# Optimization experiments

Measured on AMD Instinct MI355X. Metric: run time of the kernel, lower is better.

## Reference

```python
import jax, jax.numpy as jnp
import numpy as np

B, H_IMG, W_IMG, C_IMG, NP = 8, 384, 384, 3, 6
DELTA = 10
TOL = 1e-3
LAM = 0.05          # lambda_ (Charbonnier scale)
MAX_ITER = 12
RIDGE = 1e-6


def _cubic(s):
    # Keys bicubic convolution kernel, a = -0.5
    a = -0.5
    s = jnp.abs(s)
    s2 = s * s
    s3 = s2 * s
    w1 = (a + 2.0) * s3 - (a + 3.0) * s2 + 1.0
    w2 = a * s3 - 5.0 * a * s2 + 8.0 * a * s - 4.0 * a
    return jnp.where(s <= 1.0, w1, jnp.where(s < 2.0, w2, 0.0))


def _bicubic(I, xg, yg):
    # I: [b,H,W,C]; xg,yg: [b,H,W] sample coordinates
    Bn, Hh, Ww, C = I.shape
    x0 = jnp.floor(xg)
    y0 = jnp.floor(yg)
    tx = xg - x0
    ty = yg - y0
    xi = x0.astype(jnp.int32)
    yi = y0.astype(jnp.int32)
    bidx = jnp.arange(Bn)[:, None, None]
    out = jnp.zeros(I.shape, I.dtype)
    for j in range(4):           # fixed 4x4 tap stencil
        wy = _cubic(ty - (j - 1))
        yy = jnp.clip(yi + (j - 1), 0, Hh - 1)
        for k in range(4):
            wx = _cubic(tx - (k - 1))
            xx = jnp.clip(xi + (k - 1), 0, Ww - 1)
            out = out + (wy * wx)[..., None] * I[bidx, yy, xx, :]
    return out


def _params2matrix(p):
    # AFFINITY: x' = x + p0 + p2*x + p3*y ; y' = y + p1 + p4*x + p5*y
    zero = jnp.zeros_like(p[:, 0])
    one = jnp.ones_like(p[:, 0])
    r0 = jnp.stack([1.0 + p[:, 2], p[:, 3], p[:, 0]], -1)
    r1 = jnp.stack([p[:, 4], 1.0 + p[:, 5], p[:, 1]], -1)
    r2 = jnp.stack([zero, zero, one], -1)
    return jnp.stack([r0, r1, r2], 1)


def _matrix2params(M):
    M = M / M[:, 2:3, 2:3]
    return jnp.stack([M[:, 0, 2], M[:, 1, 2], M[:, 0, 0] - 1.0,
                      M[:, 0, 1], M[:, 1, 0], M[:, 1, 1] - 1.0], -1)


def _gradients(I):
    # central differences, zero-padded at the borders (as in compute_gradients)
    Ix = jnp.pad((I[:, :, 2:, :] - I[:, :, :-2, :]) * 0.5,
                 ((0, 0), (0, 0), (1, 1), (0, 0)))
    Iy = jnp.pad((I[:, 2:, :, :] - I[:, :-2, :, :]) * 0.5,
                 ((0, 0), (1, 1), (0, 0), (0, 0)))
    return Ix, Iy


def setup_inputs() -> dict:
    key = jax.random.key(0)
    k1, k2 = jax.random.split(key)
    I1 = jax.random.uniform(k1, (B, H_IMG, W_IMG, C_IMG), jnp.float32)
    I2 = jax.random.uniform(k2, (B, H_IMG, W_IMG, C_IMG), jnp.float32)
    p = jnp.zeros((B, NP), jnp.float32)
    return {"I1": I1, "I2": I2, "p": p}


def _forward(I1, I2, p):
    Bn, Hh, Ww, C = I1.shape
    x = jnp.arange(Ww, dtype=jnp.float32)
    y = jnp.arange(Hh, dtype=jnp.float32)
    X, Y = jnp.meshgrid(x, y)
    ones = jnp.ones_like(X)
    zeros = jnp.zeros_like(X)
    # AFFINITY Jacobian, split into Jx / Jy halves: [H,W,6]
    Jx = jnp.stack([ones, zeros, X, Y, zeros, zeros], -1)
    Jy = jnp.stack([zeros, ones, zeros, zeros, X, Y], -1)
    Ix, Iy = _gradients(I1)
    # steepest-descent images: [b,H,W,C,6]
    DIJ = Ix[..., None] * Jx[None, :, :, None, :] + Iy[..., None] * Jy[None, :, :, None, :]
    rows_ok = (jnp.arange(Hh) >= DELTA) & (jnp.arange(Hh) < Hh - DELTA)
    cols_ok = (jnp.arange(Ww) >= DELTA) & (jnp.arange(Ww) < Ww - DELTA)
    valid1 = (rows_ok[:, None] & cols_ok[None, :])[None, :, :, None]  # [1,H,W,1]
    coords = jnp.stack([X, Y, ones], 0)  # [3,H,W]
    eye = jnp.eye(NP, dtype=jnp.float32)

    def warp(pcur):
        M = _params2matrix(pcur)
        g = jnp.einsum('bij,jhw->bihw', M, coords)
        xg, yg = g[:, 0], g[:, 1]
        Iw = _bicubic(I2, xg, yg)
        gx = jnp.round(xg).astype(jnp.int32)
        gy = jnp.round(yg).astype(jnp.int32)
        wmask = ((gx >= DELTA) & (gx <= Ww - DELTA) &
                 (gy >= DELTA) & (gy <= Hh - DELTA))[..., None]
        return Iw, wmask

    def step(carry, _):
        pcur, done = carry
        Iw, wmask = carry_warp = warp(pcur)
        m = wmask & valid1
        DI = jnp.where(m, Iw - I1, 0.0)
        # Charbonnier influence weight psi(e) = 1/sqrt(1 + (e/lam)^2)
        w = jnp.where(m, jax.lax.rsqrt(1.0 + (DI / LAM) ** 2), 0.0)
        bvec = jnp.einsum('bhwcm,bhwc->bm', DIJ, w * DI)
        Hm = jnp.einsum('bhwcm,bhwcn->bmn', DIJ * w[..., None], DIJ)
        dp = jnp.linalg.solve(Hm + RIDGE * eye, bvec[..., None])[..., 0]
        # inverse-compositional update: W(p) <- W(p) o W(dp)^-1
        Mn = _params2matrix(pcur) @ jnp.linalg.inv(_params2matrix(dp))
        p_new = _matrix2params(Mn)
        conv = jnp.linalg.norm(dp, axis=-1) < TOL
        p_out = jnp.where(done[:, None], pcur, p_new)
        return (p_out, done | conv), None

    (pf, _), _ = jax.lax.scan(step, (p, jnp.zeros((Bn,), bool)), None, length=MAX_ITER)
    Iw, wmask = warp(pf)
    m = wmask & valid1
    DI = jnp.where(m, Iw - I1, 0.0)
    rho = 2.0 * LAM * LAM * (jnp.sqrt(1.0 + (DI / LAM) ** 2) - 1.0)
    mb = jnp.broadcast_to(m, DI.shape)
    cnt = jnp.sum(mb.astype(jnp.float32), axis=(1, 2, 3))
    err = jnp.sum(jnp.where(mb, rho, 0.0), axis=(1, 2, 3)) / jnp.maximum(cnt, 1.0)
    return pf, err, DI, Iw


def reference(I1, I2, p):
    return _forward(I1, I2, p)
```

## Files before the change

### kernel.cpp

```cpp
#include <hip/hip_runtime.h>
#include <math.h>

#define BB 8
#define HH 384
#define WW 384
#define NPAR 6
#define DEL 10
#define MAXIT 12
#define NACC 24
#define HWPIX (HH*WW)
#define NRT4 91
#define PITCH2 195
#define NR2 8
#define WS2C 194
#define WIN 182
#define PITCHF 141
#define WSF 140
#define KB_ 8
#define SPS 32

typedef float vf4 __attribute__((ext_vector_type(4)));
typedef vf4 uvf4 __attribute__((aligned(4)));
typedef float f2v __attribute__((ext_vector_type(2), aligned(4)));
typedef float lf4 __attribute__((ext_vector_type(4)));

__device__ __forceinline__ vf4 ldv4(const float* p) { return *(const uvf4*)p; }

__device__ __forceinline__ lf4 ldpx3(const float* __restrict__ Ib, int pixoff) {
    const int fo = pixoff * 3;
    if (fo + 4 <= HWPIX * 3) {
        vf4 v = ldv4(Ib + fo);
        return (lf4){v.x, v.y, v.z, 0.f};
    }
    vf4 v = ldv4(Ib + fo - 1);
    return (lf4){v.y, v.z, v.w, 0.f};
}

__device__ __forceinline__ float cubicw(float s) {
    s = fabsf(s);
    float s2 = s * s, s3 = s2 * s;
    float w1 = 1.5f * s3 - 2.5f * s2 + 1.0f;
    float w2 = -0.5f * s3 + 2.5f * s2 - 4.0f * s + 2.0f;
    return (s <= 1.0f) ? w1 : ((s < 2.0f) ? w2 : 0.0f);
}

__device__ __forceinline__ void bicubic3_fast(const float* __restrict__ Ib, double xg, double yg, float Iw[3]) {
    double fx = floor(xg), fy = floor(yg);
    float tx = (float)(xg - fx), ty = (float)(yg - fy);
    int xi = (int)fx, yi = (int)fy;
    float wx[4], wyv[4];
#pragma unroll
    for (int k = 0; k < 4; k++) { wx[k] = cubicw(tx - (float)(k - 1)); wyv[k] = cubicw(ty - (float)(k - 1)); }
    Iw[0] = 0.f; Iw[1] = 0.f; Iw[2] = 0.f;
    const float* base = Ib + (yi - 1) * (WW * 3) + (xi - 1) * 3;
#pragma unroll
    for (int j = 0; j < 4; j++) {
        const float* r = base + j * (WW * 3);
        vf4 v0 = ldv4(r), v1 = ldv4(r + 4), v2 = ldv4(r + 8);
        float r0 = fmaf(wx[0], v0.x, 0.f); r0 = fmaf(wx[1], v0.w, r0); r0 = fmaf(wx[2], v1.z, r0); r0 = fmaf(wx[3], v2.y, r0);
        float r1 = fmaf(wx[0], v0.y, 0.f); r1 = fmaf(wx[1], v1.x, r1); r1 = fmaf(wx[2], v1.w, r1); r1 = fmaf(wx[3], v2.z, r1);
        float r2 = fmaf(wx[0], v0.z, 0.f); r2 = fmaf(wx[1], v1.y, r2); r2 = fmaf(wx[2], v2.x, r2); r2 = fmaf(wx[3], v2.w, r2);
        Iw[0] = fmaf(wyv[j], r0, Iw[0]);
        Iw[1] = fmaf(wyv[j], r1, Iw[1]);
        Iw[2] = fmaf(wyv[j], r2, Iw[2]);
    }
}

__device__ __forceinline__ void bicubic3_gen(const float* __restrict__ Ib, double xg, double yg, float Iw[3]) {
    double fx = floor(xg), fy = floor(yg);
    int xi = (int)fx, yi = (int)fy;
    float tx = (float)(xg - fx), ty = (float)(yg - fy);
    float wx[4], wyv[4];
    int xx[4], yy[4];
#pragma unroll
    for (int k = 0; k < 4; k++) {
        wx[k] = cubicw(tx - (float)(k - 1)); wyv[k] = cubicw(ty - (float)(k - 1));
        xx[k] = min(max(xi + k - 1, 0), WW - 1);
        yy[k] = min(max(yi + k - 1, 0), HH - 1);
    }
    Iw[0] = 0.f; Iw[1] = 0.f; Iw[2] = 0.f;
#pragma unroll
    for (int j = 0; j < 4; j++) {
        const float* row = Ib + yy[j] * (WW * 3);
        float r0 = 0.f, r1 = 0.f, r2 = 0.f;
#pragma unroll
        for (int k = 0; k < 4; k++) {
            const float* q = row + xx[k] * 3;
            r0 = fmaf(wx[k], q[0], r0); r1 = fmaf(wx[k], q[1], r1); r2 = fmaf(wx[k], q[2], r2);
        }
        Iw[0] = fmaf(wyv[j], r0, Iw[0]);
        Iw[1] = fmaf(wyv[j], r1, Iw[1]);
        Iw[2] = fmaf(wyv[j], r2, Iw[2]);
    }
}

template<int P>
__device__ __forceinline__ void bicubic3_lds(const lf4* __restrict__ T, int ssx, int ssy,
                                             float tx, float ty, float Iw[3]) {
    float wx[4], wyv[4];
#pragma unroll
    for (int k = 0; k < 4; k++) { wx[k] = cubicw(tx - (float)(k - 1)); wyv[k] = cubicw(ty - (float)(k - 1)); }
    Iw[0] = 0.f; Iw[1] = 0.f; Iw[2] = 0.f;
    const lf4* bp = T + (ssy - 1) * P + (ssx - 1);
#pragma unroll
    for (int j = 0; j < 4; j++) {
        lf4 t0 = bp[j * P + 0], t1 = bp[j * P + 1], t2 = bp[j * P + 2], t3 = bp[j * P + 3];
        float r0 = fmaf(wx[0], t0.x, 0.f); r0 = fmaf(wx[1], t1.x, r0); r0 = fmaf(wx[2], t2.x, r0); r0 = fmaf(wx[3], t3.x, r0);
        float r1 = fmaf(wx[0], t0.y, 0.f); r1 = fmaf(wx[1], t1.y, r1); r1 = fmaf(wx[2], t2.y, r1); r1 = fmaf(wx[3], t3.y, r1);
        float r2 = fmaf(wx[0], t0.z, 0.f); r2 = fmaf(wx[1], t1.z, r2); r2 = fmaf(wx[2], t2.z, r2); r2 = fmaf(wx[3], t3.z, r2);
        Iw[0] = fmaf(wyv[j], r0, Iw[0]);
        Iw[1] = fmaf(wyv[j], r1, Iw[1]);
        Iw[2] = fmaf(wyv[j], r2, Iw[2]);
    }
}

__device__ __forceinline__
void solve6_fast(const double* __restrict__ Sb, const double* __restrict__ pc,
                 double pn[6], int* convp) {
    const double b0 = Sb[0], b1 = Sb[3], b2 = Sb[1], b3 = Sb[2], b4 = Sb[4], b5 = Sb[5];
    const double h00 = Sb[6]  + 1e-6, h01 = Sb[12], h02 = Sb[7],  h03 = Sb[8],  h04 = Sb[13], h05 = Sb[14];
    const double h11 = Sb[18] + 1e-6, h12 = Sb[13], h13 = Sb[14], h14 = Sb[19], h15 = Sb[20];
    const double h22 = Sb[9]  + 1e-6, h23 = Sb[10], h24 = Sb[15], h25 = Sb[16];
    const double h33 = Sb[11] + 1e-6, h34 = Sb[16], h35 = Sb[17];
    const double h44 = Sb[21] + 1e-6, h45 = Sb[22];
    const double h55 = Sb[23] + 1e-6;

    const double l00 = sqrt(h00);
    const double i0 = 1.0 / l00;
    const double l10 = h01 * i0, l20 = h02 * i0, l30 = h03 * i0, l40 = h04 * i0, l50 = h05 * i0;
    const double l11 = sqrt(h11 - l10 * l10);
    const double i1 = 1.0 / l11;
    const double l21 = (h12 - l20 * l10) * i1;
    const double l31 = (h13 - l30 * l10) * i1;
    const double l41 = (h14 - l40 * l10) * i1;
    const double l51 = (h15 - l50 * l10) * i1;
    const double l22 = sqrt(h22 - l20 * l20 - l21 * l21);
    const double i2 = 1.0 / l22;
    const double l32 = (h23 - l30 * l20 - l31 * l21) * i2;
    const double l42 = (h24 - l40 * l20 - l41 * l21) * i2;
    const double l52 = (h25 - l50 * l20 - l51 * l21) * i2;
    const double l33 = sqrt(h33 - l30 * l30 - l31 * l31 - l32 * l32);
    const double i3 = 1.0 / l33;
    const double l43 = (h34 - l40 * l30 - l41 * l31 - l42 * l32) * i3;
    const double l53 = (h35 - l50 * l30 - l51 * l31 - l52 * l32) * i3;
    const double l44 = sqrt(h44 - l40 * l40 - l41 * l41 - l42 * l42 - l43 * l43);
    const double i4 = 1.0 / l44;
    const double l54 = (h45 - l50 * l40 - l51 * l41 - l52 * l42 - l53 * l43) * i4;
    const double l55 = sqrt(h55 - l50 * l50 - l51 * l51 - l52 * l52 - l53 * l53 - l54 * l54);
    const double i5 = 1.0 / l55;

    const double y0 = b0 * i0;
    const double y1 = (b1 - l10 * y0) * i1;
    const double y2 = (b2 - l20 * y0 - l21 * y1) * i2;
    const double y3 = (b3 - l30 * y0 - l31 * y1 - l32 * y2) * i3;
    const double y4 = (b4 - l40 * y0 - l41 * y1 - l42 * y2 - l43 * y3) * i4;
    const double y5 = (b5 - l50 * y0 - l51 * y1 - l52 * y2 - l53 * y3 - l54 * y4) * i5;

    const double d5 = y5 * i5;
    const double d4 = (y4 - l54 * d5) * i4;
    const double d3 = (y3 - l43 * d4 - l53 * d5) * i3;
    const double d2 = (y2 - l32 * d3 - l42 * d4 - l52 * d5) * i2;
    const double d1 = (y1 - l21 * d2 - l31 * d3 - l41 * d4 - l51 * d5) * i1;
    const double d0 = (y0 - l10 * d1 - l20 * d2 - l30 * d3 - l40 * d4 - l50 * d5) * i0;

    const double nrm = sqrt(d0*d0 + d1*d1 + d2*d2 + d3*d3 + d4*d4 + d5*d5);
    *convp = (nrm < 1e-3) ? 1 : 0;

    const double m00 = 1.0 + pc[2], m01 = pc[3], m02 = pc[0];
    const double m10 = pc[4], m11 = 1.0 + pc[5], m12 = pc[1];
    const double q00 = 1.0 + d2, q01 = d3, q02 = d0;
    const double q10 = d4, q11 = 1.0 + d5, q12 = d1;
    const double det = q00 * q11 - q01 * q10;
    const double j00 = q11 / det, j01 = -q01 / det;
    const double j10 = -q10 / det, j11 = q00 / det;
    const double jt0 = -(j00 * q02 + j01 * q12);
    const double jt1 = -(j10 * q02 + j11 * q12);
    const double n00 = m00 * j00 + m01 * j10;
    const double n01 = m00 * j01 + m01 * j11;
    const double n02 = m00 * jt0 + m01 * jt1 + m02;
    const double n10 = m10 * j00 + m11 * j10;
    const double n11 = m10 * j01 + m11 * j11;
    const double n12 = m10 * jt0 + m11 * jt1 + m12;
    pn[0] = n02;
    pn[1] = n12;
    pn[2] = n00 - 1.0;
    pn[3] = n01;
    pn[4] = n10;
    pn[5] = n11 - 1.0;
}

extern "C" __global__ __launch_bounds__(256)
void k_init(const float* __restrict__ p0, double* __restrict__ p_store,
            int* __restrict__ done0, double* __restrict__ S_part_all,
            double* __restrict__ Sf_part) {
    const int idx = blockIdx.x * 256 + threadIdx.x;
    const int n = MAXIT * KB_ * BB * SPS;
    for (int i = idx; i < n; i += gridDim.x * 256) S_part_all[i] = 0.0;
    if (blockIdx.x == 0) {
        const int tid = threadIdx.x;
        if (tid < KB_ * BB * 4) Sf_part[tid] = 0.0;
        if (tid < BB * NPAR) p_store[tid] = (double)p0[tid];
        if (tid < BB) done0[tid] = 0;
    }
}

extern "C" __global__ __launch_bounds__(256)
void k_iter(const float* __restrict__ I1, const float* __restrict__ I2,
            const double* __restrict__ p_in, const int* __restrict__ done_in,
            const double* __restrict__ S_in, double* __restrict__ S_out,
            double* __restrict__ p_out_g, int* __restrict__ done_out_g,
            int first) {
    __shared__ lf4 SMEM[NR2 * PITCH2];
    __shared__ double Ssum[NACC];
    __shared__ double pbc[NPAR];
    __shared__ int dbc;
    const int tid = threadIdx.x;
    const int b = blockIdx.y;

    if (!first) {
        if (tid < NACC) {
            double a0 = 0.0, a1 = 0.0;
#pragma unroll
            for (int k = 0; k < KB_; k += 2) {
                a0 += S_in[((size_t)(k * BB + b)) * SPS + tid];
                a1 += S_in[((size_t)((k + 1) * BB + b)) * SPS + tid];
            }
            Ssum[tid] = a0 + a1;
        }
        __syncthreads();
    }
    if (tid == 0) {
        if (first) {
#pragma unroll
            for (int i = 0; i < NPAR; i++) pbc[i] = p_in[b * NPAR + i];
            dbc = done_in[b];
        } else {
            if (done_in[b]) {
#pragma unroll
                for (int i = 0; i < NPAR; i++) pbc[i] = p_in[b * NPAR + i];
                dbc = 1;
            } else {
                double pn[6]; int conv;
                solve6_fast(Ssum, p_in + b * NPAR, pn, &conv);
#pragma unroll
                for (int i = 0; i < NPAR; i++) pbc[i] = pn[i];
                dbc = conv;
            }
            if (blockIdx.x == 0) {
#pragma unroll
                for (int i = 0; i < NPAR; i++) p_out_g[b * NPAR + i] = pbc[i];
                done_out_g[b] = dbc;
            }
        }
    }
    __syncthreads();
    if (dbc) return;

    const int tix = blockIdx.x;
    const int rt = tix >> 1, win = tix & 1;
    const int y0 = 10 + rt * 4;
    const int x0 = 10 + win * WIN;
    const int sx0 = x0 - 6;

    const double M00 = 1.0 + pbc[2], M01 = pbc[3], M02 = pbc[0];
    const double M10 = pbc[4], M11 = 1.0 + pbc[5], M12 = pbc[1];
    const float* I1b = I1 + (size_t)b * HWPIX * 3;
    const float* I2b = I2 + (size_t)b * HWPIX * 3;

    const double ygc = M10 * (double)(x0 + 91) + M11 * ((double)y0 + 1.5) + M12;
    const int r0 = (int)fmin(fmax(floor(ygc) - 3.0, -100000.0), 100000.0);

    for (int i = tid; i < NR2 * WS2C; i += 256) {
        const int r = i / WS2C, c = i - r * WS2C;
        const int gr = min(max(r0 + r, 0), HH - 1);
        const int gc = min(sx0 + c, WW - 1);
        SMEM[r * PITCH2 + c] = ldpx3(I2b, gr * WW + gc);
    }
    __syncthreads();

    const int wid = tid >> 6, lane = tid & 63;
    const int y = y0 + wid;
    const double Y = (double)y;
    const double Bx = M01 * Y + M02;
    const double By = M11 * Y + M12;

    double s[13];
#pragma unroll
    for (int i = 0; i < 13; i++) s[i] = 0.0;

#pragma unroll
    for (int step = 0; step < 3; step++) {
        const int col = lane + 64 * step;
        const int x = x0 + col;
        const double X = (double)x;
        const double xg = fma(M00, X, Bx);
        const double yg = fma(M10, X, By);
        const double gx = rint(xg), gy = rint(yg);
        const bool ok = (col < WIN) &&
                        (gx >= (double)DEL && gx <= (double)(WW - DEL) &&
                         gy >= (double)DEL && gy <= (double)(HH - DEL));
        const double fx = floor(xg), fy = floor(yg);
        const int xi = (int)fx, yi = (int)fy;
        const float tx = (float)(xg - fx), ty = (float)(yg - fy);
        const int sxi = xi - sx0, syi = yi - r0;
        const bool inwin = ok && (sxi >= 1) && (sxi <= WS2C - 3) && (syi >= 1) && (syi <= NR2 - 3);

        float Iw[3];
        if (ok && !inwin) {
            bicubic3_fast(I2b, xg, yg, Iw);
        } else {
            const int ssx = inwin ? sxi : 8;
            const int ssy = inwin ? syi : 2;
            bicubic3_lds<PITCH2>(SMEM, ssx, ssy, tx, ty, Iw);
        }

        const int xc = min(x, WW - DEL - 1);
        const int pixL = y * WW + xc;
        const float* c = I1b + pixL * 3;
        vf4 u0 = ldv4(c - 3);
        vf4 u1 = ldv4(c + 1);
        float cr2 = c[5];
        vf4 uu = ldv4(c - WW * 3);
        vf4 ud = ldv4(c + WW * 3);

        const float cl[3] = {u0.x, u0.y, u0.z};
        const float cv[3] = {u0.w, u1.x, u1.y};
        const float cr[3] = {u1.z, u1.w, cr2};
        const float cu[3] = {uu.x, uu.y, uu.z};
        const float cd[3] = {ud.x, ud.y, ud.z};

        const float msk = ok ? 1.0f : 0.0f;
        float Af = 0.f, Bf = 0.f, Cf = 0.f, T0f = 0.f, T1f = 0.f;
#pragma unroll
        for (int ch = 0; ch < 3; ch++) {
            const float Ix = (cr[ch] - cl[ch]) * 0.5f;
            const float Iy = (cd[ch] - cu[ch]) * 0.5f;
            const float d = Iw[ch] - cv[ch];
            const float u = d * 20.0f;
            const float w = msk / sqrtf(fmaf(u, u, 1.0f));
            const float wd = w * d;
            T0f = fmaf(Ix, wd, T0f);
            T1f = fmaf(Iy, wd, T1f);
            const float wIx = w * Ix;
            Af = fmaf(wIx, Ix, Af);
            Bf = fmaf(wIx, Iy, Bf);
            Cf = fmaf(w * Iy, Iy, Cf);
        }
        const double T0 = (double)T0f, T1 = (double)T1f;
        const double A = (double)Af, Bd = (double)Bf, Cd = (double)Cf;
        const double XX = X * X;
        s[0] += T0;  s[1] = fma(T0, X, s[1]);
        s[2] += T1;  s[3] = fma(T1, X, s[3]);
        s[4] += A;   s[5] = fma(A, X, s[5]);   s[6] = fma(A, XX, s[6]);
        s[7] += Bd;  s[8] = fma(Bd, X, s[8]);  s[9] = fma(Bd, XX, s[9]);
        s[10] += Cd; s[11] = fma(Cd, X, s[11]); s[12] = fma(Cd, XX, s[12]);
    }

#pragma unroll
    for (int i = 0; i < 13; i++) s[i] += __shfl_down(s[i], 32, 64);

    __syncthreads();
    double* scr = (double*)SMEM;
    if (lane < 32) {
        double* o = scr + ((size_t)(wid * 32 + lane)) * 13;
#pragma unroll
        for (int i = 0; i < 13; i++) o[i] = s[i];
    }
    __syncthreads();

    if (tid < NACC) {
        const int comp[NACC] = {0,1,0, 2,3,2, 4,5,4, 6,5,4, 7,8,7, 9,8,7, 10,11,10, 12,11,10};
        const int ypw[NACC]  = {0,0,1, 0,0,1, 0,0,1, 0,1,2, 0,0,1, 0,1,2, 0,0,1,   0,1,2};
        const int cix = comp[tid], pw = ypw[tid];
        double acc = 0.0;
        for (int w = 0; w < 4; w++) {
            const double* basep = scr + ((size_t)(w * 32)) * 13 + cix;
            double part = 0.0;
            for (int l = 0; l < 32; l++) part += basep[(size_t)l * 13];
            const double Yw = (double)(y0 + w);
            const double f = (pw == 0) ? 1.0 : ((pw == 1) ? Yw : Yw * Yw);
            acc = fma(f, part, acc);
        }
        const int bkt = blockIdx.x & (KB_ - 1);
        unsafeAtomicAdd(&S_out[((size_t)(bkt * BB + b)) * SPS + tid], acc);
    }
}

extern "C" __global__ __launch_bounds__(256)
void k_final_map(const float* __restrict__ I1, const float* __restrict__ I2,
                 const double* __restrict__ p_in, const int* __restrict__ done_in,
                 const double* __restrict__ S_in, double* __restrict__ pf_g,
                 float* __restrict__ DI_out, float* __restrict__ Iw_out,
                 double* __restrict__ Sf_part) {
    __shared__ lf4 I2S[NR2 * PITCHF];
    __shared__ double wsum[4][2];
    __shared__ double Ssum[NACC];
    __shared__ double pbc[NPAR];
    const int tid = threadIdx.x;
    const int b = blockIdx.y;

    if (tid < NACC) {
        double a0 = 0.0, a1 = 0.0;
#pragma unroll
        for (int k = 0; k < KB_; k += 2) {
            a0 += S_in[((size_t)(k * BB + b)) * SPS + tid];
            a1 += S_in[((size_t)((k + 1) * BB + b)) * SPS + tid];
        }
        Ssum[tid] = a0 + a1;
    }
    __syncthreads();
    if (tid == 0) {
        if (done_in[b]) {
#pragma unroll
            for (int i = 0; i < NPAR; i++) pbc[i] = p_in[b * NPAR + i];
        } else {
            double pn[6]; int conv;
            solve6_fast(Ssum, p_in + b * NPAR, pn, &conv);
#pragma unroll
            for (int i = 0; i < NPAR; i++) pbc[i] = pn[i];
        }
        if (blockIdx.x == 0) {
#pragma unroll
            for (int i = 0; i < NPAR; i++) pf_g[b * NPAR + i] = pbc[i];
        }
    }
    __syncthreads();

    const int tix = blockIdx.x;
    const int rt = tix / 3, win = tix - rt * 3;
    const int y0 = rt * 4;
    const int x0 = win * 128;
    const int sx0 = x0 - 6;

    const double M00 = 1.0 + pbc[2], M01 = pbc[3], M02 = pbc[0];
    const double M10 = pbc[4], M11 = 1.0 + pbc[5], M12 = pbc[1];
    const float* I1b = I1 + (size_t)b * HWPIX * 3;
    const float* I2b = I2 + (size_t)b * HWPIX * 3;
    float* DIb = DI_out + (size_t)b * HWPIX * 3;
    float* Iwb = Iw_out + (size_t)b * HWPIX * 3;

    const double ygc = M10 * (double)(x0 + 64) + M11 * ((double)y0 + 1.5) + M12;
    const int r0 = (int)fmin(fmax(floor(ygc) - 3.0, -100000.0), 100000.0);

    for (int i = tid; i < NR2 * WSF; i += 256) {
        const int r = i / WSF, c = i - r * WSF;
        const int gr = min(max(r0 + r, 0), HH - 1);
        const int gc = min(max(sx0 + c, 0), WW - 1);
        I2S[r * PITCHF + c] = ldpx3(I2b, gr * WW + gc);
    }
    __syncthreads();

    const int row = tid >> 6, lane = tid & 63;
    const int y = y0 + row;
    const int x1 = x0 + 2 * lane;
    const int pix1 = y * WW + x1;

    float Iwp[2][3];
    bool mp[2];
    double rho_s = 0.0, cnt_s = 0.0;

    const float* cbase = I1b + (size_t)pix1 * 3;
    const vf4 Ac = ldv4(cbase);
    const vf4 A2c = ldv4(cbase + 2);

#pragma unroll
    for (int j = 0; j < 2; j++) {
        const int x = x1 + j;
        const double X = (double)x, Yd = (double)y;
        const double xg = fma(M00, X, fma(M01, Yd, M02));
        const double yg = fma(M10, X, fma(M11, Yd, M12));
        const double fx = floor(xg), fy = floor(yg);
        const int xi = (int)fx, yi = (int)fy;
        const float tx = (float)(xg - fx), ty = (float)(yg - fy);
        const int sxi = xi - sx0, syi = yi - r0;
        const bool inwin = (sxi >= 1) && (sxi <= WSF - 3) && (syi >= 1) && (syi <= NR2 - 3);

        if (inwin) bicubic3_lds<PITCHF>(I2S, sxi, syi, tx, ty, Iwp[j]);
        else       bicubic3_gen(I2b, xg, yg, Iwp[j]);

        const bool v1 = (x >= DEL) && (x < WW - DEL) && (y >= DEL) && (y < HH - DEL);
        const double gx = rint(xg), gy = rint(yg);
        const bool wm = (gx >= (double)DEL && gx <= (double)(WW - DEL) &&
                         gy >= (double)DEL && gy <= (double)(HH - DEL));
        mp[j] = v1 && wm;
    }

    {
        float* wp = Iwb + (size_t)pix1 * 3;
        *(uvf4*)wp = (vf4){Iwp[0][0], Iwp[0][1], Iwp[0][2], Iwp[1][0]};
        *(f2v*)(wp + 4) = (f2v){Iwp[1][1], Iwp[1][2]};
    }
    {
        const float cv1[3] = {Ac.x, Ac.y, Ac.z};
        const float cv2[3] = {Ac.w, A2c.z, A2c.w};
        float dv[6];
#pragma unroll
        for (int ch = 0; ch < 3; ch++) {
            const float d1 = mp[0] ? (Iwp[0][ch] - cv1[ch]) : 0.0f;
            const float d2 = mp[1] ? (Iwp[1][ch] - cv2[ch]) : 0.0f;
            dv[ch] = d1;
            dv[3 + ch] = d2;
            if (mp[0]) {
                const float u = d1 * 20.0f;
                rho_s += (double)(0.005f * (sqrtf(fmaf(u, u, 1.0f)) - 1.0f));
            }
            if (mp[1]) {
                const float u = d2 * 20.0f;
                rho_s += (double)(0.005f * (sqrtf(fmaf(u, u, 1.0f)) - 1.0f));
            }
        }
        if (mp[0]) cnt_s += 3.0;
        if (mp[1]) cnt_s += 3.0;
        float* dp_ = DIb + (size_t)pix1 * 3;
        *(uvf4*)dp_ = (vf4){dv[0], dv[1], dv[2], dv[3]};
        *(f2v*)(dp_ + 4) = (f2v){dv[4], dv[5]};
    }

#pragma unroll
    for (int off = 32; off >= 1; off >>= 1) {
        rho_s += __shfl_down(rho_s, off, 64);
        cnt_s += __shfl_down(cnt_s, off, 64);
    }
    if (lane == 0) { wsum[row][0] = rho_s; wsum[row][1] = cnt_s; }
    __syncthreads();
    if (tid < 2) {
        double sv = wsum[0][tid] + wsum[1][tid] + wsum[2][tid] + wsum[3][tid];
        const int bkt = blockIdx.x & (KB_ - 1);
        unsafeAtomicAdd(&Sf_part[((size_t)(bkt * BB + b)) * 4 + tid], sv);
    }
}

extern "C" __global__ void k_finish(const double* __restrict__ p_fin,
                                    const double* __restrict__ Sf_part,
                                    float* __restrict__ out) {
    const int tid = threadIdx.x;
    if (tid < BB * NPAR) out[tid] = (float)p_fin[tid];
    if (tid >= 48 && tid < 48 + BB) {
        const int b = tid - 48;
        double rs = 0.0, cs = 0.0;
#pragma unroll
        for (int k = 0; k < KB_; k++) {
            rs += Sf_part[((size_t)(k * BB + b)) * 4 + 0];
            cs += Sf_part[((size_t)(k * BB + b)) * 4 + 1];
        }
        out[48 + b] = (float)(rs / fmax(cs, 1.0));
    }
}

extern "C" void kernel_launch(void* const* d_in, const int* in_sizes, int n_in,
                              void* d_out, int out_size, void* d_ws, size_t ws_size,
                              hipStream_t stream) {
    const float* I1 = (const float*)d_in[0];
    const float* I2 = (const float*)d_in[1];
    const float* p0 = (const float*)d_in[2];
    float* out = (float*)d_out;

    double* p_store = (double*)d_ws;
    int* done_flags = (int*)((char*)d_ws + 4992);
    double* S_part_all = (double*)((char*)d_ws + 5408);
    double* Sf_part = (double*)((char*)d_ws + 202016);

    k_init<<<8, 256, 0, stream>>>(p0, p_store, done_flags, S_part_all, Sf_part);

    const size_t SIT = (size_t)KB_ * BB * SPS;
    dim3 gridI(NRT4 * 2, BB), blkI(256);
    for (int it = 0; it < MAXIT; it++) {
        const int first = (it == 0) ? 1 : 0;
        const double* p_in = p_store + (size_t)(first ? 0 : (it - 1)) * BB * NPAR;
        const int* d_in_f = done_flags + (first ? 0 : (it - 1)) * BB;
        const double* S_in = S_part_all + (size_t)(first ? 0 : (it - 1)) * SIT;
        k_iter<<<gridI, blkI, 0, stream>>>(I1, I2, p_in, d_in_f, S_in,
                                           S_part_all + (size_t)it * SIT,
                                           p_store + (size_t)it * BB * NPAR,
                                           done_flags + it * BB, first);
    }
    float* DI_out = out + 56;
    float* Iw_out = out + 56 + (size_t)BB * HWPIX * 3;
    dim3 gridF(96 * 3, BB), blkF(256);
    k_final_map<<<gridF, blkF, 0, stream>>>(I1, I2,
                                            p_store + (size_t)11 * BB * NPAR,
                                            done_flags + 11 * BB,
                                            S_part_all + (size_t)11 * SIT,
                                            p_store + (size_t)MAXIT * BB * NPAR,
                                            DI_out, Iw_out, Sf_part);
    k_finish<<<1, 64, 0, stream>>>(p_store + (size_t)MAXIT * BB * NPAR, Sf_part, out);
}
```

Before: 425.5 us.

## Retile iteration and final kernels to one pixel per thread, prefetch warp source early

```diff
diff --git a/kernel.cpp b/kernel.cpp
--- a/kernel.cpp
+++ b/kernel.cpp
@@ -10,10 +10,11 @@
 #define NACC 24
 #define HWPIX (HH*WW)
 #define NRT4 91
-#define PITCH2 195
 #define NR2 8
-#define WS2C 194
-#define WIN 182
+#define W_STG 76
+#define PITCH2 77
+#define NWIN 6
+#define NR2F 6
 #define PITCHF 141
 #define WSF 140
 #define KB_ 8
@@ -204,40 +205,64 @@
     }
 }
 
-extern "C" __global__ __launch_bounds__(256)
+extern "C" __global__ __launch_bounds__(256, 8)
 void k_iter(const float* __restrict__ I1, const float* __restrict__ I2,
             const double* __restrict__ p_in, const int* __restrict__ done_in,
             const double* __restrict__ S_in, double* __restrict__ S_out,
             double* __restrict__ p_out_g, int* __restrict__ done_out_g,
             int first) {
-    __shared__ lf4 SMEM[NR2 * PITCH2];
+    __shared__ __align__(16) double SMEMD[1664];
     __shared__ double Ssum[NACC];
     __shared__ double pbc[NPAR];
     __shared__ int dbc;
+    lf4* SMEM = (lf4*)SMEMD;
     const int tid = threadIdx.x;
     const int b = blockIdx.y;
-
-    if (!first) {
-        if (tid < NACC) {
-            double a0 = 0.0, a1 = 0.0;
-#pragma unroll
-            for (int k = 0; k < KB_; k += 2) {
-                a0 += S_in[((size_t)(k * BB + b)) * SPS + tid];
-                a1 += S_in[((size_t)((k + 1) * BB + b)) * SPS + tid];
-            }
-            Ssum[tid] = a0 + a1;
-        }
-        __syncthreads();
-    }
+    const int tix = blockIdx.x;
+    const int rt = tix / NWIN, win = tix - rt * NWIN;
+    const int y0 = 10 + rt * 4;
+    const int x0 = 10 + win * 64;
+    const int sx0 = x0 - 6;
+
+    double pp[NPAR];
+#pragma unroll
+    for (int i = 0; i < NPAR; i++) pp[i] = p_in[b * NPAR + i];
+    {
+        const double pM10 = pp[4], pM11 = 1.0 + pp[5], pM12 = pp[1];
+        const double ygc = pM10 * (double)(x0 + 32) + pM11 * ((double)y0 + 1.5) + pM12;
+        const int r0 = (int)fmin(fmax(floor(ygc) - 3.0, -100000.0), 100000.0);
+        const float* I2b = I2 + (size_t)b * HWPIX * 3;
+        for (int i = tid; i < NR2 * W_STG; i += 256) {
+            const int r = i / W_STG, c = i - r * W_STG;
+            const int gr = min(max(r0 + r, 0), HH - 1);
+            const int gc = min(sx0 + c, WW - 1);
+            SMEM[r * PITCH2 + c] = ldpx3(I2b, gr * WW + gc);
+        }
+    }
+    const double pM10_ = pp[4], pM11_ = 1.0 + pp[5], pM12_ = pp[1];
+    const double ygc_ = pM10_ * (double)(x0 + 32) + pM11_ * ((double)y0 + 1.5) + pM12_;
+    const int r0 = (int)fmin(fmax(floor(ygc_) - 3.0, -100000.0), 100000.0);
+
+    if (!first && tid < NACC) {
+        double a0 = 0.0, a1 = 0.0;
+#pragma unroll
+        for (int k = 0; k < KB_; k += 2) {
+            a0 += S_in[((size_t)(k * BB + b)) * SPS + tid];
+            a1 += S_in[((size_t)((k + 1) * BB + b)) * SPS + tid];
+        }
+        Ssum[tid] = a0 + a1;
+    }
+    __syncthreads();
+
     if (tid == 0) {
         if (first) {
 #pragma unroll
-            for (int i = 0; i < NPAR; i++) pbc[i] = p_in[b * NPAR + i];
+            for (int i = 0; i < NPAR; i++) pbc[i] = pp[i];
             dbc = done_in[b];
         } else {
             if (done_in[b]) {
 #pragma unroll
-                for (int i = 0; i < NPAR; i++) pbc[i] = p_in[b * NPAR + i];
+                for (int i = 0; i < NPAR; i++) pbc[i] = pp[i];
                 dbc = 1;
             } else {
                 double pn[6]; int conv;
@@ -256,27 +281,10 @@
     __syncthreads();
     if (dbc) return;
 
-    const int tix = blockIdx.x;
-    const int rt = tix >> 1, win = tix & 1;
-    const int y0 = 10 + rt * 4;
-    const int x0 = 10 + win * WIN;
-    const int sx0 = x0 - 6;
-
     const double M00 = 1.0 + pbc[2], M01 = pbc[3], M02 = pbc[0];
     const double M10 = pbc[4], M11 = 1.0 + pbc[5], M12 = pbc[1];
     const float* I1b = I1 + (size_t)b * HWPIX * 3;
     const float* I2b = I2 + (size_t)b * HWPIX * 3;
-
-    const double ygc = M10 * (double)(x0 + 91) + M11 * ((double)y0 + 1.5) + M12;
-    const int r0 = (int)fmin(fmax(floor(ygc) - 3.0, -100000.0), 100000.0);
-
-    for (int i = tid; i < NR2 * WS2C; i += 256) {
-        const int r = i / WS2C, c = i - r * WS2C;
-        const int gr = min(max(r0 + r, 0), HH - 1);
-        const int gc = min(sx0 + c, WW - 1);
-        SMEM[r * PITCH2 + c] = ldpx3(I2b, gr * WW + gc);
-    }
-    __syncthreads();
 
     const int wid = tid >> 6, lane = tid & 63;
     const int y = y0 + wid;
@@ -284,83 +292,76 @@
     const double Bx = M01 * Y + M02;
     const double By = M11 * Y + M12;
 
+    const int x = x0 + lane;
+    const double X = (double)x;
+    const double xg = fma(M00, X, Bx);
+    const double yg = fma(M10, X, By);
+    const double gx = rint(xg), gy = rint(yg);
+    const bool ok = (x < WW - DEL) &&
+                    (gx >= (double)DEL && gx <= (double)(WW - DEL) &&
+                     gy >= (double)DEL && gy <= (double)(HH - DEL));
+    const double fx = floor(xg), fy = floor(yg);
+    const int xi = (int)fx, yi = (int)fy;
+    const float tx = (float)(xg - fx), ty = (float)(yg - fy);
+    const int sxi = xi - sx0, syi = yi - r0;
+    const bool inwin = ok && (sxi >= 1) && (sxi <= W_STG - 3) && (syi >= 1) && (syi <= NR2 - 3);
+
+    float Iw[3];
+    if (ok && !inwin) {
+        bicubic3_fast(I2b, xg, yg, Iw);
+    } else {
+        const int ssx = inwin ? sxi : 8;
+        const int ssy = inwin ? syi : 2;
+        bicubic3_lds<PITCH2>(SMEM, ssx, ssy, tx, ty, Iw);
+    }
+
+    const int xc = min(x, WW - DEL - 1);
+    const int pixL = y * WW + xc;
+    const float* c = I1b + pixL * 3;
+    vf4 u0 = ldv4(c - 3);
+    vf4 u1 = ldv4(c + 1);
+    float cr2 = c[5];
+    vf4 uu = ldv4(c - WW * 3);
+    vf4 ud = ldv4(c + WW * 3);
+
+    const float cl[3] = {u0.x, u0.y, u0.z};
+    const float cv[3] = {u0.w, u1.x, u1.y};
+    const float cr[3] = {u1.z, u1.w, cr2};
+    const float cu[3] = {uu.x, uu.y, uu.z};
+    const float cd[3] = {ud.x, ud.y, ud.z};
+
+    const float msk = ok ? 1.0f : 0.0f;
+    float Af = 0.f, Bf = 0.f, Cf = 0.f, T0f = 0.f, T1f = 0.f;
+#pragma unroll
+    for (int ch = 0; ch < 3; ch++) {
+        const float Ix = (cr[ch] - cl[ch]) * 0.5f;
+        const float Iy = (cd[ch] - cu[ch]) * 0.5f;
+        const float d = Iw[ch] - cv[ch];
+        const float u = d * 20.0f;
+        const float w = msk / sqrtf(fmaf(u, u, 1.0f));
+        const float wd = w * d;
+        T0f = fmaf(Ix, wd, T0f);
+        T1f = fmaf(Iy, wd, T1f);
+        const float wIx = w * Ix;
+        Af = fmaf(wIx, Ix, Af);
+        Bf = fmaf(wIx, Iy, Bf);
+        Cf = fmaf(w * Iy, Iy, Cf);
+    }
+    const double T0 = (double)T0f, T1 = (double)T1f;
+    const double A = (double)Af, Bd = (double)Bf, Cd = (double)Cf;
+    const double XX = X * X;
     double s[13];
-#pragma unroll
-    for (int i = 0; i < 13; i++) s[i] = 0.0;
-
-#pragma unroll
-    for (int step = 0; step < 3; step++) {
-        const int col = lane + 64 * step;
-        const int x = x0 + col;
-        const double X = (double)x;
-        const double xg = fma(M00, X, Bx);
-        const double yg = fma(M10, X, By);
-        const double gx = rint(xg), gy = rint(yg);
-        const bool ok = (col < WIN) &&
-                        (gx >= (double)DEL && gx <= (double)(WW - DEL) &&
-                         gy >= (double)DEL && gy <= (double)(HH - DEL));
-        const double fx = floor(xg), fy = floor(yg);
-        const int xi = (int)fx, yi = (int)fy;
-        const float tx = (float)(xg - fx), ty = (float)(yg - fy);
-        const int sxi = xi - sx0, syi = yi - r0;
-        const bool inwin = ok && (sxi >= 1) && (sxi <= WS2C - 3) && (syi >= 1) && (syi <= NR2 - 3);
-
-        float Iw[3];
-        if (ok && !inwin) {
-            bicubic3_fast(I2b, xg, yg, Iw);
-        } else {
-            const int ssx = inwin ? sxi : 8;
-            const int ssy = inwin ? syi : 2;
-            bicubic3_lds<PITCH2>(SMEM, ssx, ssy, tx, ty, Iw);
-        }
-
-        const int xc = min(x, WW - DEL - 1);
-        const int pixL = y * WW + xc;
-        const float* c = I1b + pixL * 3;
-        vf4 u0 = ldv4(c - 3);
-        vf4 u1 = ldv4(c + 1);
-        float cr2 = c[5];
-        vf4 uu = ldv4(c - WW * 3);
-        vf4 ud = ldv4(c + WW * 3);
-
-        const float cl[3] = {u0.x, u0.y, u0.z};
-        const float cv[3] = {u0.w, u1.x, u1.y};
-        const float cr[3] = {u1.z, u1.w, cr2};
-        const float cu[3] = {uu.x, uu.y, uu.z};
-        const float cd[3] = {ud.x, ud.y, ud.z};
-
-        const float msk = ok ? 1.0f : 0.0f;
-        float Af = 0.f, Bf = 0.f, Cf = 0.f, T0f = 0.f, T1f = 0.f;
-#pragma unroll
-        for (int ch = 0; ch < 3; ch++) {
-            const float Ix = (cr[ch] - cl[ch]) * 0.5f;
-            const float Iy = (cd[ch] - cu[ch]) * 0.5f;
-            const float d = Iw[ch] - cv[ch];
-            const float u = d * 20.0f;
-            const float w = msk / sqrtf(fmaf(u, u, 1.0f));
-            const float wd = w * d;
-            T0f = fmaf(Ix, wd, T0f);
-            T1f = fmaf(Iy, wd, T1f);
-            const float wIx = w * Ix;
-            Af = fmaf(wIx, Ix, Af);
-            Bf = fmaf(wIx, Iy, Bf);
-            Cf = fmaf(w * Iy, Iy, Cf);
-        }
-        const double T0 = (double)T0f, T1 = (double)T1f;
-        const double A = (double)Af, Bd = (double)Bf, Cd = (double)Cf;
-        const double XX = X * X;
-        s[0] += T0;  s[1] = fma(T0, X, s[1]);
-        s[2] += T1;  s[3] = fma(T1, X, s[3]);
-        s[4] += A;   s[5] = fma(A, X, s[5]);   s[6] = fma(A, XX, s[6]);
-        s[7] += Bd;  s[8] = fma(Bd, X, s[8]);  s[9] = fma(Bd, XX, s[9]);
-        s[10] += Cd; s[11] = fma(Cd, X, s[11]); s[12] = fma(Cd, XX, s[12]);
-    }
+    s[0] = T0;  s[1] = T0 * X;
+    s[2] = T1;  s[3] = T1 * X;
+    s[4] = A;   s[5] = A * X;   s[6] = A * XX;
+    s[7] = Bd;  s[8] = Bd * X;  s[9] = Bd * XX;
+    s[10] = Cd; s[11] = Cd * X; s[12] = Cd * XX;
 
 #pragma unroll
     for (int i = 0; i < 13; i++) s[i] += __shfl_down(s[i], 32, 64);
 
     __syncthreads();
-    double* scr = (double*)SMEM;
+    double* scr = SMEMD;
     if (lane < 32) {
         double* o = scr + ((size_t)(wid * 32 + lane)) * 13;
 #pragma unroll
@@ -369,9 +370,11 @@
     __syncthreads();
 
     if (tid < NACC) {
-        const int comp[NACC] = {0,1,0, 2,3,2, 4,5,4, 6,5,4, 7,8,7, 9,8,7, 10,11,10, 12,11,10};
-        const int ypw[NACC]  = {0,0,1, 0,0,1, 0,0,1, 0,1,2, 0,0,1, 0,1,2, 0,0,1,   0,1,2};
-        const int cix = comp[tid], pw = ypw[tid];
+        const unsigned long long CLO = 0x9787456454232010ULL;
+        const unsigned long long CHI = 0x00000000abcaba78ULL;
+        const unsigned long long YPW = 0x0000910910910410ULL;
+        const int cix = (int)(((tid < 16) ? (CLO >> (tid * 4)) : (CHI >> ((tid - 16) * 4))) & 0xF);
+        const int pw  = (int)((YPW >> (tid * 2)) & 0x3);
         double acc = 0.0;
         for (int w = 0; w < 4; w++) {
             const double* basep = scr + ((size_t)(w * 32)) * 13 + cix;
@@ -386,19 +389,39 @@
     }
 }
 
-extern "C" __global__ __launch_bounds__(256)
+extern "C" __global__ __launch_bounds__(256, 8)
 void k_final_map(const float* __restrict__ I1, const float* __restrict__ I2,
                  const double* __restrict__ p_in, const int* __restrict__ done_in,
                  const double* __restrict__ S_in, double* __restrict__ pf_g,
                  float* __restrict__ DI_out, float* __restrict__ Iw_out,
                  double* __restrict__ Sf_part) {
-    __shared__ lf4 I2S[NR2 * PITCHF];
+    __shared__ lf4 I2S[NR2F * PITCHF];
     __shared__ double wsum[4][2];
     __shared__ double Ssum[NACC];
     __shared__ double pbc[NPAR];
     const int tid = threadIdx.x;
     const int b = blockIdx.y;
-
+    const int tix = blockIdx.x;
+    const int rt = tix / 3, win = tix - rt * 3;
+    const int y0 = rt * 2;
+    const int x0 = win * 128;
+    const int sx0 = x0 - 6;
+
+    double pp[NPAR];
+#pragma unroll
+    for (int i = 0; i < NPAR; i++) pp[i] = p_in[b * NPAR + i];
+    const double pM10 = pp[4], pM11 = 1.0 + pp[5], pM12 = pp[1];
+    const double ygc = pM10 * (double)(x0 + 64) + pM11 * ((double)y0 + 0.5) + pM12;
+    const int r0 = (int)fmin(fmax(floor(ygc) - 2.0, -100000.0), 100000.0);
+    {
+        const float* I2b = I2 + (size_t)b * HWPIX * 3;
+        for (int i = tid; i < NR2F * WSF; i += 256) {
+            const int r = i / WSF, c = i - r * WSF;
+            const int gr = min(max(r0 + r, 0), HH - 1);
+            const int gc = min(max(sx0 + c, 0), WW - 1);
+            I2S[r * PITCHF + c] = ldpx3(I2b, gr * WW + gc);
+        }
+    }
     if (tid < NACC) {
         double a0 = 0.0, a1 = 0.0;
 #pragma unroll
@@ -412,7 +435,7 @@
     if (tid == 0) {
         if (done_in[b]) {
 #pragma unroll
-            for (int i = 0; i < NPAR; i++) pbc[i] = p_in[b * NPAR + i];
+            for (int i = 0; i < NPAR; i++) pbc[i] = pp[i];
         } else {
             double pn[6]; int conv;
             solve6_fast(Ssum, p_in + b * NPAR, pn, &conv);
@@ -425,12 +448,6 @@
         }
     }
     __syncthreads();
-
-    const int tix = blockIdx.x;
-    const int rt = tix / 3, win = tix - rt * 3;
-    const int y0 = rt * 4;
-    const int x0 = win * 128;
-    const int sx0 = x0 - 6;
 
     const double M00 = 1.0 + pbc[2], M01 = pbc[3], M02 = pbc[0];
     const double M10 = pbc[4], M11 = 1.0 + pbc[5], M12 = pbc[1];
@@ -439,81 +456,55 @@
     float* DIb = DI_out + (size_t)b * HWPIX * 3;
     float* Iwb = Iw_out + (size_t)b * HWPIX * 3;
 
-    const double ygc = M10 * (double)(x0 + 64) + M11 * ((double)y0 + 1.5) + M12;
-    const int r0 = (int)fmin(fmax(floor(ygc) - 3.0, -100000.0), 100000.0);
-
-    for (int i = tid; i < NR2 * WSF; i += 256) {
-        const int r = i / WSF, c = i - r * WSF;
-        const int gr = min(max(r0 + r, 0), HH - 1);
-        const int gc = min(max(sx0 + c, 0), WW - 1);
-        I2S[r * PITCHF + c] = ldpx3(I2b, gr * WW + gc);
-    }
-    __syncthreads();
-
-    const int row = tid >> 6, lane = tid & 63;
+    const int row = tid >> 7;
+    const int x = x0 + (tid & 127);
     const int y = y0 + row;
-    const int x1 = x0 + 2 * lane;
-    const int pix1 = y * WW + x1;
-
-    float Iwp[2][3];
-    bool mp[2];
+    const int pix = y * WW + x;
+
+    const double X = (double)x, Yd = (double)y;
+    const double xg = fma(M00, X, fma(M01, Yd, M02));
+    const double yg = fma(M10, X, fma(M11, Yd, M12));
+    const double fx = floor(xg), fy = floor(yg);
+    const int xi = (int)fx, yi = (int)fy;
+    const float tx = (float)(xg - fx), ty = (float)(yg - fy);
+    const int sxi = xi - sx0, syi = yi - r0;
+    const bool inwin = (sxi >= 1) && (sxi <= WSF - 3) && (syi >= 1) && (syi <= NR2F - 3);
+
+    float Iwp[3];
+    if (inwin) bicubic3_lds<PITCHF>(I2S, sxi, syi, tx, ty, Iwp);
+    else       bicubic3_gen(I2b, xg, yg, Iwp);
+
+    const bool v1 = (x >= DEL) && (x < WW - DEL) && (y >= DEL) && (y < HH - DEL);
+    const double gx = rint(xg), gy = rint(yg);
+    const bool wm = (gx >= (double)DEL && gx <= (double)(WW - DEL) &&
+                     gy >= (double)DEL && gy <= (double)(HH - DEL));
+    const bool mp = v1 && wm;
+
+    const float* cbase = I1b + (size_t)pix * 3;
+    const float cv0 = cbase[0], cv1 = cbase[1], cv2 = cbase[2];
+
+    {
+        float* wp = Iwb + (size_t)pix * 3;
+        *(f2v*)wp = (f2v){Iwp[0], Iwp[1]};
+        wp[2] = Iwp[2];
+    }
     double rho_s = 0.0, cnt_s = 0.0;
-
-    const float* cbase = I1b + (size_t)pix1 * 3;
-    const vf4 Ac = ldv4(cbase);
-    const vf4 A2c = ldv4(cbase + 2);
-
-#pragma unroll
-    for (int j = 0; j < 2; j++) {
-        const int x = x1 + j;
-        const double X = (double)x, Yd = (double)y;
-        const double xg = fma(M00, X, fma(M01, Yd, M02));
-        const double yg = fma(M10, X, fma(M11, Yd, M12));
-        const double fx = floor(xg), fy = floor(yg);
-        const int xi = (int)fx, yi = (int)fy;
-        const float tx = (float)(xg - fx), ty = (float)(yg - fy);
-        const int sxi = xi - sx0, syi = yi - r0;
-        const bool inwin = (sxi >= 1) && (sxi <= WSF - 3) && (syi >= 1) && (syi <= NR2 - 3);
-
-        if (inwin) bicubic3_lds<PITCHF>(I2S, sxi, syi, tx, ty, Iwp[j]);
-        else       bicubic3_gen(I2b, xg, yg, Iwp[j]);
-
-        const bool v1 = (x >= DEL) && (x < WW - DEL) && (y >= DEL) && (y < HH - DEL);
-        const double gx = rint(xg), gy = rint(yg);
-        const bool wm = (gx >= (double)DEL && gx <= (double)(WW - DEL) &&
-                         gy >= (double)DEL && gy <= (double)(HH - DEL));
-        mp[j] = v1 && wm;
-    }
-
     {
-        float* wp = Iwb + (size_t)pix1 * 3;
-        *(uvf4*)wp = (vf4){Iwp[0][0], Iwp[0][1], Iwp[0][2], Iwp[1][0]};
-        *(f2v*)(wp + 4) = (f2v){Iwp[1][1], Iwp[1][2]};
-    }
-    {
-        const float cv1[3] = {Ac.x, Ac.y, Ac.z};
-        const float cv2[3] = {Ac.w, A2c.z, A2c.w};
-        float dv[6];
+        const float cvv[3] = {cv0, cv1, cv2};
+        float dv[3];
 #pragma unroll
         for (int ch = 0; ch < 3; ch++) {
-            const float d1 = mp[0] ? (Iwp[0][ch] - cv1[ch]) : 0.0f;
-            const float d2 = mp[1] ? (Iwp[1][ch] - cv2[ch]) : 0.0f;
+            const float d1 = mp ? (Iwp[ch] - cvv[ch]) : 0.0f;
             dv[ch] = d1;
-            dv[3 + ch] = d2;
-            if (mp[0]) {
+            if (mp) {
                 const float u = d1 * 20.0f;
                 rho_s += (double)(0.005f * (sqrtf(fmaf(u, u, 1.0f)) - 1.0f));
             }
-            if (mp[1]) {
-                const float u = d2 * 20.0f;
-                rho_s += (double)(0.005f * (sqrtf(fmaf(u, u, 1.0f)) - 1.0f));
-            }
-        }
-        if (mp[0]) cnt_s += 3.0;
-        if (mp[1]) cnt_s += 3.0;
-        float* dp_ = DIb + (size_t)pix1 * 3;
-        *(uvf4*)dp_ = (vf4){dv[0], dv[1], dv[2], dv[3]};
-        *(f2v*)(dp_ + 4) = (f2v){dv[4], dv[5]};
+        }
+        if (mp) cnt_s += 3.0;
+        float* dp_ = DIb + (size_t)pix * 3;
+        *(f2v*)dp_ = (f2v){dv[0], dv[1]};
+        dp_[2] = dv[2];
     }
 
 #pragma unroll
@@ -521,7 +512,8 @@
         rho_s += __shfl_down(rho_s, off, 64);
         cnt_s += __shfl_down(cnt_s, off, 64);
     }
-    if (lane == 0) { wsum[row][0] = rho_s; wsum[row][1] = cnt_s; }
+    const int wv = tid >> 6, lane = tid & 63;
+    if (lane == 0) { wsum[wv][0] = rho_s; wsum[wv][1] = cnt_s; }
     __syncthreads();
     if (tid < 2) {
         double sv = wsum[0][tid] + wsum[1][tid] + wsum[2][tid] + wsum[3][tid];
@@ -560,10 +552,10 @@
     double* S_part_all = (double*)((char*)d_ws + 5408);
     double* Sf_part = (double*)((char*)d_ws + 202016);
 
-    k_init<<<8, 256, 0, stream>>>(p0, p_store, done_flags, S_part_all, Sf_part);
+    k_init<<<32, 256, 0, stream>>>(p0, p_store, done_flags, S_part_all, Sf_part);
 
     const size_t SIT = (size_t)KB_ * BB * SPS;
-    dim3 gridI(NRT4 * 2, BB), blkI(256);
+    dim3 gridI(NRT4 * NWIN, BB), blkI(256);
     for (int it = 0; it < MAXIT; it++) {
         const int first = (it == 0) ? 1 : 0;
         const double* p_in = p_store + (size_t)(first ? 0 : (it - 1)) * BB * NPAR;
@@ -576,7 +568,7 @@
     }
     float* DI_out = out + 56;
     float* Iw_out = out + 56 + (size_t)BB * HWPIX * 3;
-    dim3 gridF(96 * 3, BB), blkF(256);
+    dim3 gridF(192 * 3, BB), blkF(256);
     k_final_map<<<gridF, blkF, 0, stream>>>(I1, I2,
                                             p_store + (size_t)11 * BB * NPAR,
                                             done_flags + 11 * BB,
```

After: 450.2 us. 1.06x slower.
